# Optimization experiments

Measured on AMD Instinct MI355X. Metric: run time of the kernel, lower is better.

Reference implementation:

```python
import jax, jax.numpy as jnp
import numpy as np

THETA = 10000.0


def apply_rope(x, theta):
    # x: [batch, heads, seq, head_dim], head_dim even
    d = x.shape[-1]
    s = x.shape[-2]
    freqs = 1.0 / (theta ** (jnp.arange(0, d, 2, dtype=jnp.float32) / d))  # [d/2]
    pos = jnp.arange(s, dtype=jnp.float32)
    ang = pos[:, None] * freqs[None, :]          # [seq, d/2]
    cos, sin = jnp.cos(ang), jnp.sin(ang)
    x_even = x[..., 0::2]
    x_odd = x[..., 1::2]
    r_even = x_even * cos - x_odd * sin
    r_odd = x_even * sin + x_odd * cos
    # interleave back: [..., seq, d/2, 2] -> [..., seq, d]
    out = jnp.stack([r_even, r_odd], axis=-1).reshape(x.shape)
    return out


def setup_inputs() -> dict:
    key = jax.random.key(0)
    ks = jax.random.split(key, 5)
    B, S, D = 2, 2048, 1024
    scale = 1.0 / np.sqrt(D)
    return {
        "x": jax.random.normal(ks[0], (B, S, D), dtype=jnp.float32),
        "q_proj_weight": jax.random.normal(ks[1], (D, D), dtype=jnp.float32) * scale,
        "k_proj_weight": jax.random.normal(ks[2], (D, D), dtype=jnp.float32) * scale,
        "v_proj_weight": jax.random.normal(ks[3], (D, D), dtype=jnp.float32) * scale,
        "o_proj_weight": jax.random.normal(ks[4], (D, D), dtype=jnp.float32) * scale,
    }


def reference(x, q_proj_weight, k_proj_weight, v_proj_weight, o_proj_weight):
    B, S, D = x.shape
    H = 16
    hd = D // H
    # projections: weight is (d_out, d_in)
    q = jnp.einsum('bsd,ed->bse', x, q_proj_weight)
    k = jnp.einsum('bsd,ed->bse', x, k_proj_weight)
    v = jnp.einsum('bsd,ed->bse', x, v_proj_weight)
    # split heads -> [B, H, S, hd]
    q = q.reshape(B, S, H, hd).transpose(0, 2, 1, 3)
    k = k.reshape(B, S, H, hd).transpose(0, 2, 1, 3)
    v = v.reshape(B, S, H, hd).transpose(0, 2, 1, 3)
    q = apply_rope(q, THETA)
    k = apply_rope(k, THETA)
    scores = jnp.einsum('bhqd,bhkd->bhqk', q, k) / jnp.sqrt(jnp.float32(hd))
    causal = jnp.tril(jnp.ones((S, S), dtype=bool))
    scores = jnp.where(causal, scores, -jnp.inf)
    attn = jax.nn.softmax(scores, axis=-1)
    out = jnp.einsum('bhqk,bhkd->bhqd', attn, v)
    out = out.transpose(0, 2, 1, 3).reshape(B, S, D)
    return jnp.einsum('bsv,dv->bsd', out, o_proj_weight)
```

## Files before the change

kernel.cpp:

```cpp
#include <hip/hip_runtime.h>
#include <hip/hip_bf16.h>
#include <stdint.h>

typedef __attribute__((ext_vector_type(4))) float f32x4;
typedef __attribute__((ext_vector_type(8))) __bf16 bf16x8;
typedef __attribute__((ext_vector_type(4))) __bf16 bf16x4;

#define DEVI __device__ __forceinline__

static constexpr int S_  = 2048;
static constexpr int D_  = 1024;
static constexpr int H_  = 16;
static constexpr int HD_ = 64;
static constexpr int M_  = 2 * S_;
static constexpr float SCL2 = 0.18033688f;

DEVI void gload_lds16(const void* gsrc, void* ldst) {
  __builtin_amdgcn_global_load_lds(
      (__attribute__((address_space(1))) void*)(void*)gsrc,
      (__attribute__((address_space(3))) void*)ldst, 16, 0, 0);
}

DEVI float fexp2(float x) {
  float r;
  asm("v_exp_f32 %0, %1" : "=v"(r) : "v"(x));
  return r;
}

__global__ __launch_bounds__(256) void cvt_all_kernel(
    const float* __restrict__ x, const float* __restrict__ wq,
    const float* __restrict__ wk, const float* __restrict__ wv,
    const float* __restrict__ wo,
    __bf16* __restrict__ xb, __bf16* __restrict__ wqb,
    __bf16* __restrict__ wkb, __bf16* __restrict__ wvb,
    __bf16* __restrict__ wob, float* __restrict__ tab) {
  int blk = blockIdx.x;
  if (blk < 8192) {
    int i = blk * 256 + threadIdx.x;
    const float* src; __bf16* dst; int off;
    if (i < (1 << 20))                      { src = x;  dst = xb;  off = 0; }
    else if (i < (1 << 20) + (1 << 18))     { src = wq; dst = wqb; off = (1 << 20); }
    else if (i < (1 << 20) + 2 * (1 << 18)) { src = wk; dst = wkb; off = (1 << 20) + (1 << 18); }
    else if (i < (1 << 20) + 3 * (1 << 18)) { src = wv; dst = wvb; off = (1 << 20) + 2 * (1 << 18); }
    else                                    { src = wo; dst = wob; off = (1 << 20) + 3 * (1 << 18); }
    int j = i - off;
    float4 v = reinterpret_cast<const float4*>(src)[j];
    bf16x4 o;
    o[0] = (__bf16)v.x; o[1] = (__bf16)v.y; o[2] = (__bf16)v.z; o[3] = (__bf16)v.w;
    reinterpret_cast<bf16x4*>(dst)[j] = o;
  } else {
    int i = (blk - 8192) * 256 + threadIdx.x;
    int s = i >> 5, f = i & 31;
    float freq = powf(10000.0f, -(float)(2 * f) / (float)HD_);
    float ang = (float)s * freq;
    tab[2 * i]     = cosf(ang);
    tab[2 * i + 1] = sinf(ang);
  }
}

__global__ __launch_bounds__(256) void gemm_qkv(
    const __bf16* __restrict__ A, const __bf16* __restrict__ W0,
    const __bf16* __restrict__ W1, const __bf16* __restrict__ W2,
    __bf16* __restrict__ Cq, __bf16* __restrict__ Ck, __bf16* __restrict__ Cvt,
    const float* __restrict__ tab) {
  __shared__ __attribute__((aligned(16))) __bf16 As[128 * 32];
  __shared__ __attribute__((aligned(16))) __bf16 Bs[128 * 32];
  const int tid  = threadIdx.x;
  const int lane = tid & 63;
  const int wv   = tid >> 6;
  const int m0 = blockIdx.x * 128;
  const int n0 = blockIdx.y * 128;
  const int z  = blockIdx.z;
  const __bf16* W = (z == 0) ? W0 : (z == 1 ? W1 : W2);
  const int wm = (wv >> 1) * 64, wn = (wv & 1) * 64;
  const int arow = lane & 15;
  const int kgrp = (lane >> 4) * 8;

  f32x4 acc[4][4];
#pragma unroll
  for (int i = 0; i < 4; i++)
#pragma unroll
    for (int j = 0; j < 4; j++) acc[i][j] = f32x4{0.f, 0.f, 0.f, 0.f};

  for (int k0 = 0; k0 < 1024; k0 += 32) {
    __syncthreads();
#pragma unroll
    for (int j = 0; j < 2; ++j) {
      int c   = (wv * 2 + j) * 64 + lane;
      int row = c >> 2;
      int kc  = (c & 3) * 8;
      gload_lds16(A + (size_t)(m0 + row) * 1024 + k0 + kc,
                  As + (size_t)(wv * 2 + j) * 512);
      gload_lds16(W + (size_t)(n0 + row) * 1024 + k0 + kc,
                  Bs + (size_t)(wv * 2 + j) * 512);
    }
    asm volatile("s_waitcnt vmcnt(0)" ::: "memory");
    __syncthreads();
    bf16x8 af[4], bw[4];
#pragma unroll
    for (int i = 0; i < 4; i++)
      af[i] = *reinterpret_cast<const bf16x8*>(As + (wm + i * 16 + arow) * 32 + kgrp);
#pragma unroll
    for (int i = 0; i < 4; i++)
      bw[i] = *reinterpret_cast<const bf16x8*>(Bs + (wn + i * 16 + arow) * 32 + kgrp);
#pragma unroll
    for (int i = 0; i < 4; i++)
#pragma unroll
      for (int j = 0; j < 4; j++)
        acc[i][j] = __builtin_amdgcn_mfma_f32_16x16x32_bf16(af[i], bw[j], acc[i][j], 0, 0, 0);
  }

  if (z == 2) {
#pragma unroll
    for (int i = 0; i < 4; i++) {
      int m = m0 + wm + i * 16 + (lane >> 4) * 4;
      int bb = m >> 11, srow = m & (S_ - 1);
#pragma unroll
      for (int j = 0; j < 4; j++) {
        int n = n0 + wn + j * 16 + arow;
        int h = n >> 6, d = n & 63;
        bf16x4 o4;
#pragma unroll
        for (int r = 0; r < 4; r++) o4[r] = (__bf16)acc[i][j][r];
        *reinterpret_cast<bf16x4*>(
            Cvt + ((size_t)(bb * H_ + h) * HD_ + d) * S_ + srow) = o4;
      }
    }
  } else {
#pragma unroll
    for (int i = 0; i < 4; i++) {
#pragma unroll
      for (int j = 0; j < 4; j++) {
#pragma unroll
        for (int r = 0; r < 4; r++) {
          int m = m0 + wm + i * 16 + (lane >> 4) * 4 + r;
          int n = n0 + wn + j * 16 + arow;
          float v = acc[i][j][r];
          int bb = m >> 11, srow = m & (S_ - 1);
          int h = n >> 6, d = n & 63;
          size_t oidx = ((size_t)(bb * H_ + h) * S_ + srow) * HD_ + d;
          float other = __shfl_xor(v, 1, 64);
          int fq = d >> 1;
          float2 cssn = *reinterpret_cast<const float2*>(tab + (srow * 32 + fq) * 2);
          float rv = (d & 1) ? (other * cssn.y + v * cssn.x)
                             : (v * cssn.x - other * cssn.y);
          if (z == 0) rv *= SCL2;
          ((z == 0) ? Cq : Ck)[oidx] = (__bf16)rv;
        }
      }
    }
  }
}

__global__ __launch_bounds__(256) void gemm_bt0(
    const __bf16* __restrict__ A, const __bf16* __restrict__ W0,
    float* __restrict__ Cf) {
  constexpr int BK = 32;
  __shared__ __attribute__((aligned(16))) __bf16 As[128 * BK];
  __shared__ __attribute__((aligned(16))) __bf16 Bs[128 * BK];
  const int tid  = threadIdx.x;
  const int lane = tid & 63;
  const int wv   = tid >> 6;
  const int m0 = blockIdx.x * 128;
  const int n0 = blockIdx.y * 128;
  const int wm = (wv >> 1) * 64, wn = (wv & 1) * 64;
  const int arow = lane & 15;
  const int kgrp = (lane >> 4) * 8;

  f32x4 acc[4][4];
#pragma unroll
  for (int i = 0; i < 4; i++)
#pragma unroll
    for (int j = 0; j < 4; j++) acc[i][j] = f32x4{0.f, 0.f, 0.f, 0.f};

  for (int k0 = 0; k0 < 1024; k0 += BK) {
    __syncthreads();
#pragma unroll
    for (int j = 0; j < 2; ++j) {
      int c   = (wv * 2 + j) * 64 + lane;
      int row = c >> 2;
      int kc  = (c & 3) * 8;
      gload_lds16(A + (size_t)(m0 + row) * 1024 + k0 + kc,
                  As + (size_t)(wv * 2 + j) * 512);
      gload_lds16(W0 + (size_t)(n0 + row) * 1024 + k0 + kc,
                  Bs + (size_t)(wv * 2 + j) * 512);
    }
    asm volatile("s_waitcnt vmcnt(0)" ::: "memory");
    __syncthreads();
    bf16x8 af[4], bw[4];
#pragma unroll
    for (int i = 0; i < 4; i++)
      af[i] = *reinterpret_cast<const bf16x8*>(As + (wm + i * 16 + arow) * BK + kgrp);
#pragma unroll
    for (int i = 0; i < 4; i++)
      bw[i] = *reinterpret_cast<const bf16x8*>(Bs + (wn + i * 16 + arow) * BK + kgrp);
#pragma unroll
    for (int i = 0; i < 4; i++)
#pragma unroll
      for (int j = 0; j < 4; j++)
        acc[i][j] = __builtin_amdgcn_mfma_f32_16x16x32_bf16(af[i], bw[j], acc[i][j], 0, 0, 0);
  }

#pragma unroll
  for (int i = 0; i < 4; i++)
#pragma unroll
    for (int j = 0; j < 4; j++)
#pragma unroll
      for (int r = 0; r < 4; r++) {
        int m = m0 + wm + i * 16 + (lane >> 4) * 4 + r;
        int n = n0 + wn + j * 16 + arow;
        Cf[(size_t)m * D_ + n] = acc[i][j][r];
      }
}

__global__ __launch_bounds__(256) void attn_kernel(
    const __bf16* __restrict__ Q, const __bf16* __restrict__ K,
    const __bf16* __restrict__ Vt, __bf16* __restrict__ O) {
  __shared__ __attribute__((aligned(16))) __bf16 Ks[2][64 * 64];
  __shared__ __attribute__((aligned(16))) __bf16 Vs[2][64 * 64];
  const int tid = threadIdx.x, lane = tid & 63, wv = tid >> 6;
  const int bh = blockIdx.x;
  const int pr = blockIdx.y;
  const int b = bh >> 4, h = bh & 15;
  const __bf16* Qb  = Q  + (size_t)bh * S_ * HD_;
  const __bf16* Kb  = K  + (size_t)bh * S_ * HD_;
  const __bf16* Vtb = Vt + (size_t)bh * HD_ * S_;
  const int arow = lane & 15, g = lane >> 4;

#define STAGE(K0, BK_, BV_)                                                   \
  do {                                                                        \
    _Pragma("unroll") for (int j = 0; j < 2; ++j) {                           \
      int G = (wv * 2 + j) * 64 + lane;                                       \
      int row = G >> 3, qq = G & 7;                                           \
      int qs = qq ^ (row & 7);                                                \
      int ctp = row >> 4, rw = row & 15;                                      \
      int kph = ((ctp >> 1) << 5) + ((rw >> 2) << 3) + ((ctp & 1) << 2)       \
                + (rw & 3);                                                   \
      gload_lds16(Kb + (size_t)((K0) + kph) * HD_ + qs * 8,                   \
                  (BK_) + (wv * 2 + j) * 512);                                \
      gload_lds16(Vtb + (size_t)row * S_ + (K0) + qs * 8,                     \
                  (BV_) + (wv * 2 + j) * 512);                                \
    }                                                                         \
  } while (0)

  for (int seg = 0; seg < 2; ++seg) {
    const int qt = (seg == 0) ? pr : 31 - pr;
    const int q0 = qt * 64;
    const int nkv = qt + 1;
    const int qw = q0 + wv * 16;
    const int qg = qw + arow;

    bf16x8 aq[2];
#pragma unroll
    for (int j = 0; j < 2; j++)
      aq[j] = *reinterpret_cast<const bf16x8*>(
          Qb + (size_t)(qw + arow) * HD_ + j * 32 + g * 8);

    f32x4 po[4];
#pragma unroll
    for (int dt = 0; dt < 4; dt++) po[dt] = f32x4{0.f, 0.f, 0.f, 0.f};
    float mrow = -1e30f, lrow = 0.f;

    STAGE(0, Ks[0], Vs[0]);
    {
      int t1 = (nkv > 1) ? 64 : 0;
      STAGE(t1, Ks[1], Vs[1]);
    }
    asm volatile("s_waitcnt vmcnt(4)" ::: "memory");
    __builtin_amdgcn_s_barrier();

    for (int kt = 0; kt < nkv; ++kt) {
      const int k0 = kt * 64;
      const int cur = kt & 1;
      const __bf16* Kc = Ks[cur];
      const __bf16* Vc = Vs[cur];

      f32x4 sc4[4];
      __builtin_amdgcn_s_setprio(1);
#pragma unroll
      for (int ct = 0; ct < 4; ct++) {
        sc4[ct] = f32x4{0.f, 0.f, 0.f, 0.f};
        int L = ct * 16 + arow;
#pragma unroll
        for (int j2 = 0; j2 < 2; j2++) {
          int byt = (L * 128 + j2 * 64 + g * 16) ^ ((L & 7) << 4);
          bf16x8 kb = *reinterpret_cast<const bf16x8*>((const char*)Kc + byt);
          sc4[ct] = __builtin_amdgcn_mfma_f32_16x16x32_bf16(kb, aq[j2], sc4[ct], 0, 0, 0);
        }
      }
      __builtin_amdgcn_s_setprio(0);

      const bool full = (kt < nkv - 1);
      if (!full) {
#pragma unroll
        for (int ct = 0; ct < 4; ct++) {
          int kb0 = k0 + ((ct >> 1) << 5) + ((ct & 1) << 2) + g * 8;
#pragma unroll
          for (int r = 0; r < 4; r++)
            if (kb0 + r > qg) sc4[ct][r] = -1e30f;
        }
      }

      float mx = -1e30f;
#pragma unroll
      for (int ct = 0; ct < 4; ct++)
#pragma unroll
        for (int r = 0; r < 4; r++) mx = fmaxf(mx, sc4[ct][r]);
      mx = fmaxf(mx, __shfl_xor(mx, 16, 64));
      mx = fmaxf(mx, __shfl_xor(mx, 32, 64));

      bool noskip = !__all(mx <= mrow + 11.0f);
      if (noskip) {
        float mnew = fmaxf(mrow, mx);
        float corr = fexp2(mrow - mnew);
        mrow = mnew;
        lrow *= corr;
#pragma unroll
        for (int dt = 0; dt < 4; dt++)
#pragma unroll
          for (int r = 0; r < 4; r++) po[dt][r] *= corr;
      }

      float rs = 0.f;
      float pv[4][4];
#pragma unroll
      for (int ct = 0; ct < 4; ct++)
#pragma unroll
        for (int r = 0; r < 4; r++) {
          float e = fexp2(sc4[ct][r] - mrow);
          pv[ct][r] = e;
          rs += e;
        }
      rs += __shfl_xor(rs, 16, 64);
      rs += __shfl_xor(rs, 32, 64);
      lrow += rs;

      bf16x8 pb[2];
#pragma unroll
      for (int j2 = 0; j2 < 2; j2++) {
#pragma unroll
        for (int r = 0; r < 4; r++) {
          pb[j2][r]     = (__bf16)pv[2 * j2][r];
          pb[j2][4 + r] = (__bf16)pv[2 * j2 + 1][r];
        }
      }

      __builtin_amdgcn_s_setprio(1);
#pragma unroll
      for (int dt = 0; dt < 4; dt++) {
        int d = dt * 16 + arow;
#pragma unroll
        for (int j2 = 0; j2 < 2; j2++) {
          int byv = (d * 128 + j2 * 64 + g * 16) ^ ((d & 7) << 4);
          bf16x8 vb = *reinterpret_cast<const bf16x8*>((const char*)Vc + byv);
          po[dt] = __builtin_amdgcn_mfma_f32_16x16x32_bf16(vb, pb[j2], po[dt], 0, 0, 0);
        }
      }
      __builtin_amdgcn_s_setprio(0);

      __builtin_amdgcn_s_barrier();
      if (kt < nkv - 1) {
        int nx = kt + 2;
        if (nx > nkv - 1) nx = nkv - 1;
        STAGE(nx * 64, Ks[cur], Vs[cur]);
        asm volatile("s_waitcnt vmcnt(4)" ::: "memory");
      } else {
        asm volatile("s_waitcnt vmcnt(0)" ::: "memory");
      }
      __builtin_amdgcn_s_barrier();
    }

    float inv = __builtin_amdgcn_rcpf(lrow);
#pragma unroll
    for (int dt = 0; dt < 4; dt++) {
      bf16x4 o4;
#pragma unroll
      for (int r = 0; r < 4; r++) o4[r] = (__bf16)(po[dt][r] * inv);
      *reinterpret_cast<bf16x4*>(
          O + (size_t)(b * S_ + qg) * D_ + h * HD_ + dt * 16 + g * 4) = o4;
    }
  }
#undef STAGE
}

extern "C" void kernel_launch(void* const* d_in, const int* in_sizes, int n_in,
                              void* d_out, int out_size, void* d_ws, size_t ws_size,
                              hipStream_t stream) {
  const float* x  = (const float*)d_in[0];
  const float* wq = (const float*)d_in[1];
  const float* wk = (const float*)d_in[2];
  const float* wv = (const float*)d_in[3];
  const float* wo = (const float*)d_in[4];
  float* out = (float*)d_out;

  char* w = (char*)d_ws;
  __bf16* xb  = (__bf16*)(w);
  __bf16* wqb = (__bf16*)(w + (8u  << 20));
  __bf16* wkb = (__bf16*)(w + (10u << 20));
  __bf16* wvb = (__bf16*)(w + (12u << 20));
  __bf16* wob = (__bf16*)(w + (14u << 20));
  __bf16* qws = (__bf16*)(w + (16u << 20));
  __bf16* kws = (__bf16*)(w + (24u << 20));
  __bf16* vtw = (__bf16*)(w + (32u << 20));
  __bf16* aws = (__bf16*)(w + (40u << 20));
  float*  tab = (float*)(w + (48u << 20));

  cvt_all_kernel<<<8448, 256, 0, stream>>>(x, wq, wk, wv, wo,
                                           xb, wqb, wkb, wvb, wob, tab);
  gemm_qkv<<<dim3(32, 8, 3), 256, 0, stream>>>(xb, wqb, wkb, wvb,
                                               qws, kws, vtw, tab);
  attn_kernel<<<dim3(2 * H_, S_ / 128), 256, 0, stream>>>(qws, kws, vtw, aws);
  gemm_bt0<<<dim3(M_ / 128, D_ / 128), 256, 0, stream>>>(aws, wob, out);
}
```

Before: 125.8 us.

## Double attention KV tile to 128 keys per iteration and set occupancy hint

The attention kernel now processes 128 keys per inner iteration instead of 64. It doubles the K/V shared-memory staging buffers, rewrites the swizzled load index mapping, and widens the score, softmax and PV loops to 8 score tiles. This halves the number of loop iterations, barriers and online-softmax rescales per query tile. In exchange, LDS use per block doubles, register pressure rises, and diagonal tiles for even query tiles compute extra fully masked keys. A launch-bounds minimum of 2 blocks per CU is added to cap registers.

Measured after the change: 120.0 us. -4.6%, faster.

```diff
diff --git a/kernel.cpp b/kernel.cpp
--- a/kernel.cpp
+++ b/kernel.cpp
@@ -213,11 +213,11 @@
       }
 }
 
-__global__ __launch_bounds__(256) void attn_kernel(
+__global__ __launch_bounds__(256, 2) void attn_kernel(
     const __bf16* __restrict__ Q, const __bf16* __restrict__ K,
     const __bf16* __restrict__ Vt, __bf16* __restrict__ O) {
-  __shared__ __attribute__((aligned(16))) __bf16 Ks[2][64 * 64];
-  __shared__ __attribute__((aligned(16))) __bf16 Vs[2][64 * 64];
+  __shared__ __attribute__((aligned(16))) __bf16 Ks[2][128 * 64];
+  __shared__ __attribute__((aligned(16))) __bf16 Vs[2][64 * 128];
   const int tid = threadIdx.x, lane = tid & 63, wv = tid >> 6;
   const int bh = blockIdx.x;
   const int pr = blockIdx.y;
@@ -229,24 +229,26 @@
 
 #define STAGE(K0, BK_, BV_)                                                   \
   do {                                                                        \
-    _Pragma("unroll") for (int j = 0; j < 2; ++j) {                           \
-      int G = (wv * 2 + j) * 64 + lane;                                       \
-      int row = G >> 3, qq = G & 7;                                           \
-      int qs = qq ^ (row & 7);                                                \
-      int ctp = row >> 4, rw = row & 15;                                      \
-      int kph = ((ctp >> 1) << 5) + ((rw >> 2) << 3) + ((ctp & 1) << 2)       \
-                + (rw & 3);                                                   \
-      gload_lds16(Kb + (size_t)((K0) + kph) * HD_ + qs * 8,                   \
-                  (BK_) + (wv * 2 + j) * 512);                                \
-      gload_lds16(Vtb + (size_t)row * S_ + (K0) + qs * 8,                     \
-                  (BV_) + (wv * 2 + j) * 512);                                \
+    _Pragma("unroll") for (int j = 0; j < 4; ++j) {                           \
+      int c = (wv * 4 + j) * 64 + lane;                    \
+      int rowk = c >> 3, qqk = c & 7;                                         \
+      int qsk = qqk ^ (rowk & 7);                                             \
+      int ctp = rowk >> 4, rw = rowk & 15;                                    \
+      int kph = ((ctp & 4) << 4) + ((ctp & 2) << 4) + ((ctp & 1) << 2)        \
+                + ((rw >> 2) << 3) + (rw & 3);                                \
+      gload_lds16(Kb + (size_t)((K0) + kph) * HD_ + qsk * 8,                  \
+                  (BK_) + (size_t)(wv * 4 + j) * 512);                        \
+      int rowv = c >> 4, qqv = c & 15;                                        \
+      int qsv = qqv ^ (rowv & 7);                                             \
+      gload_lds16(Vtb + (size_t)rowv * S_ + (K0) + qsv * 8,                   \
+                  (BV_) + (size_t)(wv * 4 + j) * 512);                        \
     }                                                                         \
   } while (0)
 
   for (int seg = 0; seg < 2; ++seg) {
     const int qt = (seg == 0) ? pr : 31 - pr;
     const int q0 = qt * 64;
-    const int nkv = qt + 1;
+    const int nkv = (qt >> 1) + 1;
     const int qw = q0 + wv * 16;
     const int qg = qw + arow;
 
@@ -263,22 +265,22 @@
 
     STAGE(0, Ks[0], Vs[0]);
     {
-      int t1 = (nkv > 1) ? 64 : 0;
+      int t1 = (nkv > 1) ? 128 : 0;
       STAGE(t1, Ks[1], Vs[1]);
     }
-    asm volatile("s_waitcnt vmcnt(4)" ::: "memory");
+    asm volatile("s_waitcnt vmcnt(8)" ::: "memory");
     __builtin_amdgcn_s_barrier();
 
     for (int kt = 0; kt < nkv; ++kt) {
-      const int k0 = kt * 64;
+      const int k0 = kt * 128;
       const int cur = kt & 1;
       const __bf16* Kc = Ks[cur];
       const __bf16* Vc = Vs[cur];
 
-      f32x4 sc4[4];
+      f32x4 sc4[8];
       __builtin_amdgcn_s_setprio(1);
 #pragma unroll
-      for (int ct = 0; ct < 4; ct++) {
+      for (int ct = 0; ct < 8; ct++) {
         sc4[ct] = f32x4{0.f, 0.f, 0.f, 0.f};
         int L = ct * 16 + arow;
 #pragma unroll
@@ -290,11 +292,10 @@
       }
       __builtin_amdgcn_s_setprio(0);
 
-      const bool full = (kt < nkv - 1);
-      if (!full) {
-#pragma unroll
-        for (int ct = 0; ct < 4; ct++) {
-          int kb0 = k0 + ((ct >> 1) << 5) + ((ct & 1) << 2) + g * 8;
+      if (kt == nkv - 1) {
+#pragma unroll
+        for (int ct = 0; ct < 8; ct++) {
+          int kb0 = k0 + ((ct & 4) << 4) + ((ct & 2) << 4) + ((ct & 1) << 2) + g * 8;
 #pragma unroll
           for (int r = 0; r < 4; r++)
             if (kb0 + r > qg) sc4[ct][r] = -1e30f;
@@ -303,7 +304,7 @@
 
       float mx = -1e30f;
 #pragma unroll
-      for (int ct = 0; ct < 4; ct++)
+      for (int ct = 0; ct < 8; ct++)
 #pragma unroll
         for (int r = 0; r < 4; r++) mx = fmaxf(mx, sc4[ct][r]);
       mx = fmaxf(mx, __shfl_xor(mx, 16, 64));
@@ -322,38 +323,39 @@
       }
 
       float rs = 0.f;
-      float pv[4][4];
-#pragma unroll
-      for (int ct = 0; ct < 4; ct++)
+#pragma unroll
+      for (int ct = 0; ct < 8; ct++)
 #pragma unroll
         for (int r = 0; r < 4; r++) {
           float e = fexp2(sc4[ct][r] - mrow);
-          pv[ct][r] = e;
+          sc4[ct][r] = e;
           rs += e;
         }
       rs += __shfl_xor(rs, 16, 64);
       rs += __shfl_xor(rs, 32, 64);
       lrow += rs;
 
-      bf16x8 pb[2];
-#pragma unroll
-      for (int j2 = 0; j2 < 2; j2++) {
-#pragma unroll
-        for (int r = 0; r < 4; r++) {
-          pb[j2][r]     = (__bf16)pv[2 * j2][r];
-          pb[j2][4 + r] = (__bf16)pv[2 * j2 + 1][r];
-        }
-      }
+      bf16x8 pb[4];
+#pragma unroll
+      for (int h2 = 0; h2 < 2; h2++)
+#pragma unroll
+        for (int j2 = 0; j2 < 2; j2++) {
+#pragma unroll
+          for (int r = 0; r < 4; r++) {
+            pb[h2 * 2 + j2][r]     = (__bf16)sc4[h2 * 4 + 2 * j2][r];
+            pb[h2 * 2 + j2][4 + r] = (__bf16)sc4[h2 * 4 + 2 * j2 + 1][r];
+          }
+        }
 
       __builtin_amdgcn_s_setprio(1);
 #pragma unroll
       for (int dt = 0; dt < 4; dt++) {
         int d = dt * 16 + arow;
 #pragma unroll
-        for (int j2 = 0; j2 < 2; j2++) {
-          int byv = (d * 128 + j2 * 64 + g * 16) ^ ((d & 7) << 4);
+        for (int jj = 0; jj < 4; jj++) {
+          int byv = (d * 256 + jj * 64 + g * 16) ^ ((d & 7) << 4);
           bf16x8 vb = *reinterpret_cast<const bf16x8*>((const char*)Vc + byv);
-          po[dt] = __builtin_amdgcn_mfma_f32_16x16x32_bf16(vb, pb[j2], po[dt], 0, 0, 0);
+          po[dt] = __builtin_amdgcn_mfma_f32_16x16x32_bf16(vb, pb[jj], po[dt], 0, 0, 0);
         }
       }
       __builtin_amdgcn_s_setprio(0);
@@ -362,8 +364,8 @@
       if (kt < nkv - 1) {
         int nx = kt + 2;
         if (nx > nkv - 1) nx = nkv - 1;
-        STAGE(nx * 64, Ks[cur], Vs[cur]);
-        asm volatile("s_waitcnt vmcnt(4)" ::: "memory");
+        STAGE(nx * 128, Ks[cur], Vs[cur]);
+        asm volatile("s_waitcnt vmcnt(8)" ::: "memory");
       } else {
         asm volatile("s_waitcnt vmcnt(0)" ::: "memory");
       }
```
